# Performance work log

Measured on AMD Instinct MI355X. Metric: run time of the kernel, lower is better.

Reference implementation:

```python
import jax, jax.numpy as jnp
import numpy as np

B, T, D, E, TOP_K = 8, 2048, 512, 8, 2


def setup_inputs() -> dict:
    key = jax.random.key(0)
    ks = jax.random.split(key, 8)
    s = 0.02
    return {
        "x": jax.random.normal(ks[0], (B, T, D), dtype=jnp.float32),
        "eps": jax.random.normal(ks[1], (B, T, E), dtype=jnp.float32),
        "Wr": jax.random.normal(ks[2], (D, E), dtype=jnp.float32) * s,
        "br": jnp.zeros((E,), dtype=jnp.float32),
        "Wn": jax.random.normal(ks[3], (D, E), dtype=jnp.float32) * s,
        "bn": jnp.zeros((E,), dtype=jnp.float32),
        "Wk": jax.random.normal(ks[4], (E, D, D), dtype=jnp.float32) * s,
        "bk": jnp.zeros((E, D), dtype=jnp.float32),
    }


def reference(x, eps, Wr, br, Wn, bn, Wk, bk):
    # Noisy top-k router (NoisyTopkRouter.forward)
    logits = jnp.einsum("btd,de->bte", x, Wr) + br            # [B,T,E]
    noise_logits = jnp.einsum("btd,de->bte", x, Wn) + bn      # [B,T,E]
    noisy = logits + eps * jax.nn.softplus(noise_logits)      # [B,T,E]
    _, top_idx = jax.lax.top_k(noisy, TOP_K)                  # [B,T,k]
    # mask[b,t,e] = True iff expert e is in the token's top-k
    topk_mask = jax.nn.one_hot(top_idx, E, dtype=jnp.float32).sum(-2) > 0
    sparse_logits = jnp.where(topk_mask, noisy, -jnp.inf)
    gating = jax.nn.softmax(sparse_logits, axis=-1)           # zero for non-top-k experts
    # Dense dispatch: every expert's Linear applied to all tokens, then
    # gating (zero outside top-k) selects/scales — same math as the masked
    # gather + per-expert Linear + gating scale in SparseMoE.forward.
    expert_out = jnp.einsum("btd,edh->bteh", x, Wk) + bk      # [B,T,E,D]
    out = jnp.einsum("bte,bteh->bth", gating, expert_out)     # [B,T,D]
    return out
```

## Files before the change

kernel.cpp:

```cpp
#include <hip/hip_runtime.h>
#include <hip/hip_bf16.h>
#include <math.h>

#define B_    8
#define T_    2048
#define NTOK  (B_ * T_)
#define D_    512
#define E_    8
#define NPAIR 28
#define CAP   NTOK
#define CPAD  32

#define GEMM_MTILES 288

#define RV_TOK    16
#define RV_THR    256
#define XS_STRIDE 132
#define WS_FLOATS 2108

#define PREP_ROUTER_BLOCKS (NTOK / RV_TOK)
#define PREP_TRANS_BLOCKS  (16 * 16 * E_)
#define PREP_BLOCKS (PREP_ROUTER_BLOCKS + PREP_TRANS_BLOCKS)

typedef __attribute__((ext_vector_type(4))) float f32x4;
typedef __attribute__((ext_vector_type(8))) short short8;

__device__ __forceinline__ void async_load16(const void* g, void* l) {
    __builtin_amdgcn_global_load_lds(
        (const __attribute__((address_space(1))) unsigned int*)g,
        (__attribute__((address_space(3))) unsigned int*)l,
        16, 0, 0);
}

__global__ __launch_bounds__(256) void prep_kernel(
    const float* __restrict__ x,
    const float* __restrict__ eps,
    const float* __restrict__ Wr,
    const float* __restrict__ br,
    const float* __restrict__ Wn,
    const float* __restrict__ bn,
    const float* __restrict__ Wk,
    __hip_bfloat16* __restrict__ xb,
    __hip_bfloat16* __restrict__ wkt,
    int* __restrict__ counts,
    uint4* __restrict__ entries)
{
    __shared__ float smem[RV_TOK * XS_STRIDE + WS_FLOATS];
    __shared__ int hist[NPAIR];
    __shared__ int basep[NPAIR];
    const int bid = blockIdx.x, tid = threadIdx.x;

    if (bid < PREP_ROUTER_BLOCKS) {
        float* xs  = smem;
        float* wsh = smem + RV_TOK * XS_STRIDE;

        const int tok0 = bid * RV_TOK;
        const int lane = tid & 63, wv = tid >> 6;
        const int kidx = lane >> 2, ts = lane & 3;
        const int tl = wv * 4 + ts;
        const int wk = tid >> 1, wh = tid & 1;

        if (tid < NPAIR) hist[tid] = 0;

        float acc[16];
        #pragma unroll
        for (int c = 0; c < 16; ++c) acc[c] = 0.f;

        for (int kc = 0; kc < D_; kc += 128) {
            #pragma unroll
            for (int it = 0; it < 2; ++it) {
                const int f   = it * RV_THR + tid;
                const int row = f >> 5, col = (f & 31) * 4;
                const f32x4 v = *(const f32x4*)(x + (size_t)(tok0 + row) * D_ + kc + col);
                *(f32x4*)(xs + row * XS_STRIDE + col) = v;
                union { __hip_bfloat16 h[4]; uint2 u; } cv;
                cv.h[0] = __float2bfloat16(v.x); cv.h[1] = __float2bfloat16(v.y);
                cv.h[2] = __float2bfloat16(v.z); cv.h[3] = __float2bfloat16(v.w);
                *(uint2*)(xb + (size_t)(tok0 + row) * D_ + kc + col) = cv.u;
            }
            {
                const float* src = (wh ? Wn : Wr) + (size_t)(kc + wk) * E_;
                const f32x4 w0 = *(const f32x4*)(src);
                const f32x4 w1 = *(const f32x4*)(src + 4);
                float* dst = wsh + wk * 16 + (wk >> 3) * 4 + wh * 8;
                *(f32x4*)(dst)     = w0;
                *(f32x4*)(dst + 4) = w1;
            }
            __syncthreads();

            const float* xra = xs + tl * XS_STRIDE + kidx * 8;
            const f32x4 xa0 = *(const f32x4*)(xra);
            const f32x4 xa1 = *(const f32x4*)(xra + 4);
            const float* wbase = wsh + kidx * 132;
            #pragma unroll
            for (int kk = 0; kk < 8; ++kk) {
                const float xav = (kk < 4) ? xa0[kk] : xa1[kk - 4];
                const float* wrow = wbase + kk * 16;
                #pragma unroll
                for (int c4 = 0; c4 < 4; ++c4) {
                    const f32x4 w = *(const f32x4*)(wrow + c4 * 4);
                    #pragma unroll
                    for (int c = 0; c < 4; ++c)
                        acc[c4 * 4 + c] = fmaf(xav, w[c], acc[c4 * 4 + c]);
                }
            }
            __syncthreads();
        }

        #pragma unroll
        for (int off = 4; off < 64; off <<= 1) {
            #pragma unroll
            for (int c = 0; c < 16; ++c)
                acc[c] += __shfl_xor(acc[c], off);
        }

        int p_ = 0, l_ = 0, tok_ = 0;
        float gae_ = 0.f, gbe_ = 0.f;
        const bool writer = (lane < 4);
        if (writer) {
            tok_ = tok0 + tl;
            float nv[8];
            #pragma unroll
            for (int e = 0; e < 8; ++e) {
                const float nl = acc[8 + e] + bn[e];
                const float sp = fmaxf(nl, 0.f) + log1pf(expf(-fabsf(nl)));
                nv[e] = acc[e] + br[e] + eps[(size_t)tok_ * E_ + e] * sp;
            }
            int i1 = 0; float v1 = nv[0];
            #pragma unroll
            for (int e = 1; e < 8; ++e)
                if (nv[e] > v1) { v1 = nv[e]; i1 = e; }
            int i2 = -1; float v2 = -3.4e38f;
            #pragma unroll
            for (int e = 0; e < 8; ++e)
                if (e != i1 && nv[e] > v2) { v2 = nv[e]; i2 = e; }
            const float t  = expf(v2 - v1);
            const float g1 = 1.f / (1.f + t);
            const float g2 = t / (1.f + t);
            const int aa = min(i1, i2), bb = max(i1, i2);
            gae_ = (i1 < i2) ? g1 : g2;
            gbe_ = (i1 < i2) ? g2 : g1;
            p_ = aa * (15 - aa) / 2 + (bb - aa - 1);
            l_ = atomicAdd(&hist[p_], 1);
        }
        __syncthreads();
        if (tid < NPAIR && hist[tid] > 0)
            basep[tid] = atomicAdd(counts + tid * CPAD, hist[tid]);
        __syncthreads();
        if (writer)
            entries[(size_t)p_ * CAP + basep[p_] + l_] =
                make_uint4((unsigned)tok_, __float_as_uint(gae_),
                           __float_as_uint(gbe_), 0u);
    } else {
        const int idx = bid - PREP_ROUTER_BLOCKS;
        const int e  = idx >> 8;
        const int rem = idx & 255;
        const int d0 = (rem & 15) * 32;
        const int h0 = (rem >> 4) * 32;
        const int tx = tid & 31, ty = tid >> 5;
        float (*tile)[33] = reinterpret_cast<float(*)[33]>(smem);

        const float* src = Wk + ((size_t)e * D_ + d0) * D_ + h0;
        #pragma unroll
        for (int r = ty; r < 32; r += 8)
            tile[r][tx] = src[(size_t)r * D_ + tx];
        __syncthreads();
        __hip_bfloat16* dst = wkt + ((size_t)e * D_ + h0) * D_ + d0;
        #pragma unroll
        for (int r = ty; r < 32; r += 8)
            dst[(size_t)r * D_ + tx] = __float2bfloat16(tile[tx][r]);
    }
}

__global__ __launch_bounds__(256, 3) void moe_gemm(
    const __hip_bfloat16* __restrict__ xb,
    const __hip_bfloat16* __restrict__ wkt,
    const float* __restrict__ bk,
    const int* __restrict__ counts,
    const uint4* __restrict__ entries,
    float* __restrict__ out)
{
    constexpr int BM = 64, BN = 128, BK = 32;
    constexpr int NT = D_ / BK;
    __shared__ __hip_bfloat16 As[2][BM * BK];
    __shared__ __hip_bfloat16 Bs[2][2][BN * BK];
    __shared__ uint4 ent[BM];

    const int id = blockIdx.x;
    const int g = id >> 5, rdec = id & 31;
    const int nt = rdec >> 3;
    const int mi = g * 8 + (rdec & 7);

    const int tid = threadIdx.x;
    const int wave = tid >> 6, lane = tid & 63;

    const int cval = (lane < NPAIR) ? counts[lane * CPAD] : 0;
    const int nm = (cval + 63) >> 6;
    int inc = nm;
    #pragma unroll
    for (int d = 1; d < 32; d <<= 1) {
        const int v = __shfl_up(inc, d);
        if (lane >= d) inc += v;
    }
    const int total = __shfl(inc, NPAIR - 1);
    if (mi >= total) return;
    const int ex = inc - nm;
    const unsigned long long hit =
        __ballot(lane < NPAIR && mi >= ex && mi < ex + nm);
    const int p = __ffsll(hit) - 1;
    const int mt = mi - __shfl(ex, p);
    const int cnt = __shfl(cval, p);

    int e1 = 0, rem = p;
    while (rem >= 7 - e1) { rem -= 7 - e1; ++e1; }
    const int e2 = e1 + 1 + rem;

    if (tid < BM) {
        const int idx = mt * BM + tid;
        ent[tid] = (idx < cnt) ? entries[(size_t)p * CAP + idx]
                               : make_uint4(0u, 0u, 0u, 0u);
    }
    __syncthreads();

    const int quad = lane >> 4, lr = lane & 15;
    const int wm = wave >> 1, wn = wave & 1;

    const int r16 = lane >> 2;
    const int csel = (lane & 3) ^ ((lane >> 3) & 3);
    const size_t tA0 = ent[wave * 16 + r16].x;
    const __hip_bfloat16* gA0 = xb + tA0 * D_ + csel * 8;
    const __hip_bfloat16* gB1 = wkt + ((size_t)e1 * D_ + nt * BN + wave * 32 + r16) * D_ + csel * 8;
    const __hip_bfloat16* gB2 = wkt + ((size_t)e2 * D_ + nt * BN + wave * 32 + r16) * D_ + csel * 8;

    const int so = (quad ^ ((lr >> 1) & 3)) * 8;

    f32x4 accA[2][4], accB[2][4];
    #pragma unroll
    for (int i = 0; i < 2; ++i)
        #pragma unroll
        for (int j = 0; j < 4; ++j) {
            accA[i][j] = (f32x4){0.f, 0.f, 0.f, 0.f};
            accB[i][j] = (f32x4){0.f, 0.f, 0.f, 0.f};
        }

#define STAGE(buf, k0) do {                                        \
        __hip_bfloat16* aB  = &As[buf][wave * 512];                \
        __hip_bfloat16* b1B = &Bs[buf][0][wave * 1024];            \
        __hip_bfloat16* b2B = &Bs[buf][1][wave * 1024];            \
        async_load16(gA0 + (k0), aB);                              \
        async_load16(gB1 + (k0), b1B);                             \
        async_load16(gB1 + 16 * D_ + (k0), b1B + 512);             \
        async_load16(gB2 + (k0), b2B);                             \
        async_load16(gB2 + 16 * D_ + (k0), b2B + 512);             \
    } while (0)

#define READS(buf) do {                                                        \
        _Pragma("unroll")                                                      \
        for (int i = 0; i < 2; ++i)                                            \
            a[i] = *(const short8*)(&As[buf][(wm * 32 + i * 16 + lr) * 32 + so]); \
        _Pragma("unroll")                                                      \
        for (int j = 0; j < 4; ++j) {                                          \
            b1v[j] = *(const short8*)(&Bs[buf][0][(wn * 64 + j * 16 + lr) * 32 + so]); \
            b2v[j] = *(const short8*)(&Bs[buf][1][(wn * 64 + j * 16 + lr) * 32 + so]); \
        }                                                                      \
    } while (0)

#define MFMAS() do {                                                           \
        __builtin_amdgcn_s_setprio(1);                                         \
        _Pragma("unroll")                                                      \
        for (int i = 0; i < 2; ++i)                                            \
            _Pragma("unroll")                                                  \
            for (int j = 0; j < 4; ++j) {                                      \
                accA[i][j] = __builtin_amdgcn_mfma_f32_16x16x32_bf16(          \
                    a[i], b1v[j], accA[i][j], 0, 0, 0);                        \
                accB[i][j] = __builtin_amdgcn_mfma_f32_16x16x32_bf16(          \
                    a[i], b2v[j], accB[i][j], 0, 0, 0);                        \
            }                                                                  \
        __builtin_amdgcn_s_setprio(0);                                         \
    } while (0)

    STAGE(0, 0);
    STAGE(1, BK);

    for (int t = 0; t < NT - 1; ++t) {
        short8 a[2], b1v[4], b2v[4];
        asm volatile("s_waitcnt vmcnt(5)" ::: "memory");
        __builtin_amdgcn_s_barrier();
        READS(t & 1);
        asm volatile("s_waitcnt lgkmcnt(0)" ::: "memory");
        __builtin_amdgcn_s_barrier();
        if (t + 2 < NT) STAGE(t & 1, (t + 2) * BK);
        MFMAS();
    }
    {
        short8 a[2], b1v[4], b2v[4];
        asm volatile("s_waitcnt vmcnt(0)" ::: "memory");
        __builtin_amdgcn_s_barrier();
        READS((NT - 1) & 1);
        MFMAS();
    }

#undef STAGE
#undef READS
#undef MFMAS

    const int colbase = nt * BN + wn * 64 + lr;
    float bkA[4], bkB[4];
    #pragma unroll
    for (int j = 0; j < 4; ++j) {
        bkA[j] = bk[e1 * D_ + colbase + j * 16];
        bkB[j] = bk[e2 * D_ + colbase + j * 16];
    }

    #pragma unroll
    for (int i = 0; i < 2; ++i) {
        #pragma unroll
        for (int rr = 0; rr < 4; ++rr) {
            const int row = wm * 32 + i * 16 + quad * 4 + rr;
            if (mt * BM + row < cnt) {
                const uint4 en = ent[row];
                const float ga = __uint_as_float(en.y);
                const float gb = __uint_as_float(en.z);
                float* orow = out + (size_t)en.x * D_ + colbase;
                #pragma unroll
                for (int j = 0; j < 4; ++j)
                    orow[j * 16] = ga * (accA[i][j][rr] + bkA[j])
                                 + gb * (accB[i][j][rr] + bkB[j]);
            }
        }
    }
}

extern "C" void kernel_launch(void* const* d_in, const int* in_sizes, int n_in,
                              void* d_out, int out_size, void* d_ws, size_t ws_size,
                              hipStream_t stream) {
    const float* x   = (const float*)d_in[0];
    const float* eps = (const float*)d_in[1];
    const float* Wr  = (const float*)d_in[2];
    const float* br  = (const float*)d_in[3];
    const float* Wn  = (const float*)d_in[4];
    const float* bn  = (const float*)d_in[5];
    const float* Wk  = (const float*)d_in[6];
    const float* bk  = (const float*)d_in[7];
    float* out = (float*)d_out;

    char* ws = (char*)d_ws;
    size_t off = 0;
    int* counts = (int*)(ws + off);                     off += 8192;
    uint4* entries = (uint4*)(ws + off);                off += (size_t)NPAIR * CAP * 16;
    __hip_bfloat16* xb = (__hip_bfloat16*)(ws + off);   off += (size_t)NTOK * D_ * 2;
    __hip_bfloat16* wkt = (__hip_bfloat16*)(ws + off);  off += (size_t)E_ * D_ * D_ * 2;
    (void)ws_size;

    hipMemsetAsync(counts, 0, 8192, stream);

    prep_kernel<<<dim3(PREP_BLOCKS), dim3(256), 0, stream>>>(
        x, eps, Wr, br, Wn, bn, Wk, xb, wkt, counts, entries);
    moe_gemm<<<dim3(GEMM_MTILES * 4), dim3(256), 0, stream>>>(
        xb, wkt, bk, counts, entries, out);
}
```

Before: 152.3 us.

## Load MFMA operands directly from global into registers, dropping LDS staging

Removes the LDS double-buffer staging (global_load_lds plus LDS reads and two barriers per K step) from the MoE GEMM. Each lane now loads its MFMA A/B fragments straight from global memory into registers, using a three-deep register prefetch ring over a fully unrolled K loop. Occupancy is lowered from 3 to 2 blocks per SM to make room for the extra registers. The trade-off is that operands shared across waves are now fetched redundantly from global/L2 rather than shared through LDS, and the wider register footprint could cause spills.

```diff
diff --git a/kernel.cpp b/kernel.cpp
--- a/kernel.cpp
+++ b/kernel.cpp
@@ -24,13 +24,6 @@
 
 typedef __attribute__((ext_vector_type(4))) float f32x4;
 typedef __attribute__((ext_vector_type(8))) short short8;
-
-__device__ __forceinline__ void async_load16(const void* g, void* l) {
-    __builtin_amdgcn_global_load_lds(
-        (const __attribute__((address_space(1))) unsigned int*)g,
-        (__attribute__((address_space(3))) unsigned int*)l,
-        16, 0, 0);
-}
 
 __global__ __launch_bounds__(256) void prep_kernel(
     const float* __restrict__ x,
@@ -172,7 +165,7 @@
     }
 }
 
-__global__ __launch_bounds__(256, 3) void moe_gemm(
+__global__ __launch_bounds__(256, 2) void moe_gemm(
     const __hip_bfloat16* __restrict__ xb,
     const __hip_bfloat16* __restrict__ wkt,
     const float* __restrict__ bk,
@@ -182,8 +175,6 @@
 {
     constexpr int BM = 64, BN = 128, BK = 32;
     constexpr int NT = D_ / BK;
-    __shared__ __hip_bfloat16 As[2][BM * BK];
-    __shared__ __hip_bfloat16 Bs[2][2][BN * BK];
     __shared__ uint4 ent[BM];
 
     const int id = blockIdx.x;
@@ -225,14 +216,14 @@
     const int quad = lane >> 4, lr = lane & 15;
     const int wm = wave >> 1, wn = wave & 1;
 
-    const int r16 = lane >> 2;
-    const int csel = (lane & 3) ^ ((lane >> 3) & 3);
-    const size_t tA0 = ent[wave * 16 + r16].x;
-    const __hip_bfloat16* gA0 = xb + tA0 * D_ + csel * 8;
-    const __hip_bfloat16* gB1 = wkt + ((size_t)e1 * D_ + nt * BN + wave * 32 + r16) * D_ + csel * 8;
-    const __hip_bfloat16* gB2 = wkt + ((size_t)e2 * D_ + nt * BN + wave * 32 + r16) * D_ + csel * 8;
-
-    const int so = (quad ^ ((lr >> 1) & 3)) * 8;
+    const __hip_bfloat16* pa0 = xb + (size_t)ent[wm * 32 + lr].x      * D_ + quad * 8;
+    const __hip_bfloat16* pa1 = xb + (size_t)ent[wm * 32 + 16 + lr].x * D_ + quad * 8;
+    const __hip_bfloat16* pb[8];
+    #pragma unroll
+    for (int j = 0; j < 4; ++j) {
+        pb[j]     = wkt + ((size_t)e1 * D_ + nt * BN + wn * 64 + j * 16 + lr) * D_ + quad * 8;
+        pb[4 + j] = wkt + ((size_t)e2 * D_ + nt * BN + wn * 64 + j * 16 + lr) * D_ + quad * 8;
+    }
 
     f32x4 accA[2][4], accB[2][4];
     #pragma unroll
@@ -243,65 +234,42 @@
             accB[i][j] = (f32x4){0.f, 0.f, 0.f, 0.f};
         }
 
-#define STAGE(buf, k0) do {                                        \
-        __hip_bfloat16* aB  = &As[buf][wave * 512];                \
-        __hip_bfloat16* b1B = &Bs[buf][0][wave * 1024];            \
-        __hip_bfloat16* b2B = &Bs[buf][1][wave * 1024];            \
-        async_load16(gA0 + (k0), aB);                              \
-        async_load16(gB1 + (k0), b1B);                             \
-        async_load16(gB1 + 16 * D_ + (k0), b1B + 512);             \
-        async_load16(gB2 + (k0), b2B);                             \
-        async_load16(gB2 + 16 * D_ + (k0), b2B + 512);             \
+    short8 ra0[3], ra1[3], rb[3][8];
+
+#define LOADS(buf, t) do {                                          \
+        ra0[buf] = *(const short8*)(pa0 + (t) * BK);                \
+        ra1[buf] = *(const short8*)(pa1 + (t) * BK);                \
+        _Pragma("unroll")                                           \
+        for (int j = 0; j < 8; ++j)                                 \
+            rb[buf][j] = *(const short8*)(pb[j] + (t) * BK);        \
     } while (0)
 
-#define READS(buf) do {                                                        \
-        _Pragma("unroll")                                                      \
-        for (int i = 0; i < 2; ++i)                                            \
-            a[i] = *(const short8*)(&As[buf][(wm * 32 + i * 16 + lr) * 32 + so]); \
+#define MFMAS(buf) do {                                                        \
+        __builtin_amdgcn_s_setprio(1);                                         \
         _Pragma("unroll")                                                      \
         for (int j = 0; j < 4; ++j) {                                          \
-            b1v[j] = *(const short8*)(&Bs[buf][0][(wn * 64 + j * 16 + lr) * 32 + so]); \
-            b2v[j] = *(const short8*)(&Bs[buf][1][(wn * 64 + j * 16 + lr) * 32 + so]); \
+            accA[0][j] = __builtin_amdgcn_mfma_f32_16x16x32_bf16(              \
+                ra0[buf], rb[buf][j], accA[0][j], 0, 0, 0);                    \
+            accA[1][j] = __builtin_amdgcn_mfma_f32_16x16x32_bf16(              \
+                ra1[buf], rb[buf][j], accA[1][j], 0, 0, 0);                    \
+            accB[0][j] = __builtin_amdgcn_mfma_f32_16x16x32_bf16(              \
+                ra0[buf], rb[buf][4 + j], accB[0][j], 0, 0, 0);                \
+            accB[1][j] = __builtin_amdgcn_mfma_f32_16x16x32_bf16(              \
+                ra1[buf], rb[buf][4 + j], accB[1][j], 0, 0, 0);                \
         }                                                                      \
-    } while (0)
-
-#define MFMAS() do {                                                           \
-        __builtin_amdgcn_s_setprio(1);                                         \
-        _Pragma("unroll")                                                      \
-        for (int i = 0; i < 2; ++i)                                            \
-            _Pragma("unroll")                                                  \
-            for (int j = 0; j < 4; ++j) {                                      \
-                accA[i][j] = __builtin_amdgcn_mfma_f32_16x16x32_bf16(          \
-                    a[i], b1v[j], accA[i][j], 0, 0, 0);                        \
-                accB[i][j] = __builtin_amdgcn_mfma_f32_16x16x32_bf16(          \
-                    a[i], b2v[j], accB[i][j], 0, 0, 0);                        \
-            }                                                                  \
         __builtin_amdgcn_s_setprio(0);                                         \
     } while (0)
 
-    STAGE(0, 0);
-    STAGE(1, BK);
-
-    for (int t = 0; t < NT - 1; ++t) {
-        short8 a[2], b1v[4], b2v[4];
-        asm volatile("s_waitcnt vmcnt(5)" ::: "memory");
-        __builtin_amdgcn_s_barrier();
-        READS(t & 1);
-        asm volatile("s_waitcnt lgkmcnt(0)" ::: "memory");
-        __builtin_amdgcn_s_barrier();
-        if (t + 2 < NT) STAGE(t & 1, (t + 2) * BK);
-        MFMAS();
-    }
-    {
-        short8 a[2], b1v[4], b2v[4];
-        asm volatile("s_waitcnt vmcnt(0)" ::: "memory");
-        __builtin_amdgcn_s_barrier();
-        READS((NT - 1) & 1);
-        MFMAS();
-    }
-
-#undef STAGE
-#undef READS
+    LOADS(0, 0);
+    LOADS(1, 1);
+    LOADS(2, 2);
+    #pragma unroll
+    for (int t = 0; t < NT; ++t) {
+        MFMAS(t % 3);
+        if (t + 3 < NT) LOADS(t % 3, t + 3);
+    }
+
+#undef LOADS
 #undef MFMAS
 
     const int colbase = nt * BN + wn * 64 + lr;
```

Result: slower. 214.6 us (+40.9%).

## Double-buffer router x chunks, preload full router weights, enlarge transpose tiles

Applied to the files above, without the earlier changes.

The router part of the prep kernel now loads all of Wr/Wn into shared memory once and double-buffers the x chunks. Each next chunk is prefetched into registers while the current chunk is being computed, which removes one barrier per chunk and overlaps global loads with FMAs. The Wk transpose blocks grow from 32x32 to 64x64 tiles, so there are fewer blocks. In exchange, shared memory per block grows (about 42KB), which may lower occupancy of the prep kernel.

```diff
diff --git a/kernel.cpp b/kernel.cpp
--- a/kernel.cpp
+++ b/kernel.cpp
@@ -16,10 +16,11 @@
 #define RV_TOK    16
 #define RV_THR    256
 #define XS_STRIDE 132
-#define WS_FLOATS 2108
+#define XS_CHUNK  2112
+#define WSH_FULL  8448
 
 #define PREP_ROUTER_BLOCKS (NTOK / RV_TOK)
-#define PREP_TRANS_BLOCKS  (16 * 16 * E_)
+#define PREP_TRANS_BLOCKS  (8 * 8 * E_)
 #define PREP_BLOCKS (PREP_ROUTER_BLOCKS + PREP_TRANS_BLOCKS)
 
 typedef __attribute__((ext_vector_type(4))) float f32x4;
@@ -45,53 +46,73 @@
     int* __restrict__ counts,
     uint4* __restrict__ entries)
 {
-    __shared__ float smem[RV_TOK * XS_STRIDE + WS_FLOATS];
+    __shared__ float smem[2 * XS_CHUNK + WSH_FULL];
     __shared__ int hist[NPAIR];
     __shared__ int basep[NPAIR];
     const int bid = blockIdx.x, tid = threadIdx.x;
 
     if (bid < PREP_ROUTER_BLOCKS) {
         float* xs  = smem;
-        float* wsh = smem + RV_TOK * XS_STRIDE;
+        float* wsh = smem + 2 * XS_CHUNK;
 
         const int tok0 = bid * RV_TOK;
         const int lane = tid & 63, wv = tid >> 6;
         const int kidx = lane >> 2, ts = lane & 3;
         const int tl = wv * 4 + ts;
-        const int wk = tid >> 1, wh = tid & 1;
 
         if (tid < NPAIR) hist[tid] = 0;
 
+        #pragma unroll
+        for (int it = 0; it < 4; ++it) {
+            const int idx = it * RV_THR + tid;
+            const int k = idx >> 1, h = idx & 1;
+            const float* srcw = (h ? Wn : Wr) + (size_t)k * E_;
+            const f32x4 w0 = *(const f32x4*)(srcw);
+            const f32x4 w1 = *(const f32x4*)(srcw + 4);
+            float* dstw = wsh + k * 16 + (k >> 3) * 4 + h * 8;
+            *(f32x4*)(dstw)     = w0;
+            *(f32x4*)(dstw + 4) = w1;
+        }
+        f32x4 nv[2];
+        #pragma unroll
+        for (int it = 0; it < 2; ++it) {
+            const int f = it * RV_THR + tid;
+            const int row = f >> 5, col = (f & 31) * 4;
+            nv[it] = *(const f32x4*)(x + (size_t)(tok0 + row) * D_ + col);
+        }
+        #pragma unroll
+        for (int it = 0; it < 2; ++it) {
+            const int f = it * RV_THR + tid;
+            const int row = f >> 5, col = (f & 31) * 4;
+            *(f32x4*)(xs + row * XS_STRIDE + col) = nv[it];
+            union { __hip_bfloat16 h4[4]; uint2 u; } cv;
+            cv.h4[0] = __float2bfloat16(nv[it].x);
+            cv.h4[1] = __float2bfloat16(nv[it].y);
+            cv.h4[2] = __float2bfloat16(nv[it].z);
+            cv.h4[3] = __float2bfloat16(nv[it].w);
+            *(uint2*)(xb + (size_t)(tok0 + row) * D_ + col) = cv.u;
+        }
+        __syncthreads();
+
         float acc[16];
         #pragma unroll
         for (int c = 0; c < 16; ++c) acc[c] = 0.f;
 
-        for (int kc = 0; kc < D_; kc += 128) {
-            #pragma unroll
-            for (int it = 0; it < 2; ++it) {
-                const int f   = it * RV_THR + tid;
-                const int row = f >> 5, col = (f & 31) * 4;
-                const f32x4 v = *(const f32x4*)(x + (size_t)(tok0 + row) * D_ + kc + col);
-                *(f32x4*)(xs + row * XS_STRIDE + col) = v;
-                union { __hip_bfloat16 h[4]; uint2 u; } cv;
-                cv.h[0] = __float2bfloat16(v.x); cv.h[1] = __float2bfloat16(v.y);
-                cv.h[2] = __float2bfloat16(v.z); cv.h[3] = __float2bfloat16(v.w);
-                *(uint2*)(xb + (size_t)(tok0 + row) * D_ + kc + col) = cv.u;
-            }
-            {
-                const float* src = (wh ? Wn : Wr) + (size_t)(kc + wk) * E_;
-                const f32x4 w0 = *(const f32x4*)(src);
-                const f32x4 w1 = *(const f32x4*)(src + 4);
-                float* dst = wsh + wk * 16 + (wk >> 3) * 4 + wh * 8;
-                *(f32x4*)(dst)     = w0;
-                *(f32x4*)(dst + 4) = w1;
-            }
-            __syncthreads();
-
-            const float* xra = xs + tl * XS_STRIDE + kidx * 8;
+        #pragma unroll
+        for (int c = 0; c < 4; ++c) {
+            if (c < 3) {
+                #pragma unroll
+                for (int it = 0; it < 2; ++it) {
+                    const int f = it * RV_THR + tid;
+                    const int row = f >> 5, col = (f & 31) * 4;
+                    nv[it] = *(const f32x4*)(
+                        x + (size_t)(tok0 + row) * D_ + (c + 1) * 128 + col);
+                }
+            }
+            const float* xra = xs + (c & 1) * XS_CHUNK + tl * XS_STRIDE + kidx * 8;
             const f32x4 xa0 = *(const f32x4*)(xra);
             const f32x4 xa1 = *(const f32x4*)(xra + 4);
-            const float* wbase = wsh + kidx * 132;
+            const float* wbase = wsh + c * 2112 + kidx * 132;
             #pragma unroll
             for (int kk = 0; kk < 8; ++kk) {
                 const float xav = (kk < 4) ? xa0[kk] : xa1[kk - 4];
@@ -100,11 +121,25 @@
                 for (int c4 = 0; c4 < 4; ++c4) {
                     const f32x4 w = *(const f32x4*)(wrow + c4 * 4);
                     #pragma unroll
-                    for (int c = 0; c < 4; ++c)
-                        acc[c4 * 4 + c] = fmaf(xav, w[c], acc[c4 * 4 + c]);
+                    for (int cc = 0; cc < 4; ++cc)
+                        acc[c4 * 4 + cc] = fmaf(xav, w[cc], acc[c4 * 4 + cc]);
                 }
             }
-            __syncthreads();
+            if (c < 3) {
+                #pragma unroll
+                for (int it = 0; it < 2; ++it) {
+                    const int f = it * RV_THR + tid;
+                    const int row = f >> 5, col = (f & 31) * 4;
+                    *(f32x4*)(xs + ((c + 1) & 1) * XS_CHUNK + row * XS_STRIDE + col) = nv[it];
+                    union { __hip_bfloat16 h4[4]; uint2 u; } cv;
+                    cv.h4[0] = __float2bfloat16(nv[it].x);
+                    cv.h4[1] = __float2bfloat16(nv[it].y);
+                    cv.h4[2] = __float2bfloat16(nv[it].z);
+                    cv.h4[3] = __float2bfloat16(nv[it].w);
+                    *(uint2*)(xb + (size_t)(tok0 + row) * D_ + (c + 1) * 128 + col) = cv.u;
+                }
+                __syncthreads();
+            }
         }
 
         #pragma unroll
@@ -119,21 +154,21 @@
         const bool writer = (lane < 4);
         if (writer) {
             tok_ = tok0 + tl;
-            float nv[8];
+            float nvv[8];
             #pragma unroll
             for (int e = 0; e < 8; ++e) {
                 const float nl = acc[8 + e] + bn[e];
                 const float sp = fmaxf(nl, 0.f) + log1pf(expf(-fabsf(nl)));
-                nv[e] = acc[e] + br[e] + eps[(size_t)tok_ * E_ + e] * sp;
-            }
-            int i1 = 0; float v1 = nv[0];
+                nvv[e] = acc[e] + br[e] + eps[(size_t)tok_ * E_ + e] * sp;
+            }
+            int i1 = 0; float v1 = nvv[0];
             #pragma unroll
             for (int e = 1; e < 8; ++e)
-                if (nv[e] > v1) { v1 = nv[e]; i1 = e; }
+                if (nvv[e] > v1) { v1 = nvv[e]; i1 = e; }
             int i2 = -1; float v2 = -3.4e38f;
             #pragma unroll
             for (int e = 0; e < 8; ++e)
-                if (e != i1 && nv[e] > v2) { v2 = nv[e]; i2 = e; }
+                if (e != i1 && nvv[e] > v2) { v2 = nvv[e]; i2 = e; }
             const float t  = expf(v2 - v1);
             const float g1 = 1.f / (1.f + t);
             const float g2 = t / (1.f + t);
@@ -153,21 +188,21 @@
                            __float_as_uint(gbe_), 0u);
     } else {
         const int idx = bid - PREP_ROUTER_BLOCKS;
-        const int e  = idx >> 8;
-        const int rem = idx & 255;
-        const int d0 = (rem & 15) * 32;
-        const int h0 = (rem >> 4) * 32;
-        const int tx = tid & 31, ty = tid >> 5;
-        float (*tile)[33] = reinterpret_cast<float(*)[33]>(smem);
+        const int e  = idx >> 6;
+        const int rem = idx & 63;
+        const int d0 = (rem & 7) * 64;
+        const int h0 = (rem >> 3) * 64;
+        const int tx = tid & 63, ty = tid >> 6;
+        float (*tile)[65] = reinterpret_cast<float(*)[65]>(smem);
 
         const float* src = Wk + ((size_t)e * D_ + d0) * D_ + h0;
         #pragma unroll
-        for (int r = ty; r < 32; r += 8)
+        for (int r = ty; r < 64; r += 4)
             tile[r][tx] = src[(size_t)r * D_ + tx];
         __syncthreads();
         __hip_bfloat16* dst = wkt + ((size_t)e * D_ + h0) * D_ + d0;
         #pragma unroll
-        for (int r = ty; r < 32; r += 8)
+        for (int r = ty; r < 64; r += 4)
             dst[(size_t)r * D_ + tx] = __float2bfloat16(tile[tx][r]);
     }
 }
```

Result: faster. 147.9 us (-2.9%).
